# Kernel tuning notes

Measured on AMD Instinct MI355X. Metric: run time of the kernel, lower is better.

The kernel has to match this reference:

```python
import jax, jax.numpy as jnp
import numpy as np

B, IN_DIM, LATENT_DIM, EMBED_DIM = 262144, 512, 128, 10000


def setup_inputs() -> dict:
    key = jax.random.key(0)
    k_x, k_y, k_wlv, k_blv, k_wmu, k_bmu, k_we, k_be = jax.random.split(key, 8)
    s_in = 1.0 / np.sqrt(IN_DIM)
    s_e = 1.0 / np.sqrt(EMBED_DIM)
    return {
        "x": jax.random.normal(k_x, (B, IN_DIM), dtype=jnp.float32),
        "y": jax.random.randint(k_y, (B,), 0, EMBED_DIM, dtype=jnp.int32),
        # torch nn.Linear weights are [out_features, in_features]
        "W_logvar": jax.random.uniform(k_wlv, (LATENT_DIM, IN_DIM), minval=-s_in, maxval=s_in, dtype=jnp.float32),
        "b_logvar": jax.random.uniform(k_blv, (LATENT_DIM,), minval=-s_in, maxval=s_in, dtype=jnp.float32),
        "W_mean": jax.random.uniform(k_wmu, (LATENT_DIM, IN_DIM), minval=-s_in, maxval=s_in, dtype=jnp.float32),
        "b_mean": jax.random.uniform(k_bmu, (LATENT_DIM,), minval=-s_in, maxval=s_in, dtype=jnp.float32),
        "W_embed": jax.random.uniform(k_we, (LATENT_DIM, EMBED_DIM), minval=-s_e, maxval=s_e, dtype=jnp.float32),
        "b_embed": jax.random.uniform(k_be, (LATENT_DIM,), minval=-s_e, maxval=s_e, dtype=jnp.float32),
    }


def reference(x, y, W_logvar, b_logvar, W_mean, b_mean, W_embed, b_embed):
    # logvar / mean heads: plain dense GEMMs, x @ W.T + b
    logvar = jnp.einsum("bi,li->bl", x, W_logvar) + b_logvar
    mean = jnp.einsum("bi,li->bl", x, W_mean) + b_mean
    # one_hot(y) @ W_embed.T + b_embed  ==  gather columns of W_embed at y
    embed = jnp.take(W_embed, y, axis=1).T + b_embed  # [B, latent_dim]
    return (logvar, mean, embed)
```

## Files before the change

### kernel.cpp

```cpp
#include <hip/hip_runtime.h>
#include <hip/hip_bf16.h>

#define NB 262144
#define KD 512
#define ED 10000

typedef __attribute__((ext_vector_type(8))) short s8v;
typedef __attribute__((ext_vector_type(4))) float f4v;

typedef __attribute__((address_space(1))) const unsigned int gu32_t;
typedef __attribute__((address_space(3))) unsigned int lu32_t;

__device__ __forceinline__ short f2bf(float f) {
  union { __hip_bfloat16 h; short s; } u;
  u.h = __float2bfloat16(f);
  return u.s;
}

__global__ void prep_w(const float* __restrict__ Wlv, const float* __restrict__ Wmu,
                       unsigned short* __restrict__ wbf) {
  int i = blockIdx.x * 256 + threadIdx.x;
  int row = i >> 9, col = i & 511;
  float v = (row < 128) ? Wlv[(row << 9) | col] : Wmu[((row - 128) << 9) | col];
  union { __hip_bfloat16 h; unsigned short s; } u;
  u.h = __float2bfloat16(v);
  wbf[i] = u.s;
}

__global__ void prep_embT(const float* __restrict__ We, const float* __restrict__ be,
                          float* __restrict__ embT) {
  int v = blockIdx.x;
  int l = threadIdx.x;
  embT[(size_t)v * 128 + l] = We[(size_t)l * ED + v] + be[l];
}

__global__ __launch_bounds__(512, 4) void gemm_heads(
    const float* __restrict__ x, const unsigned short* __restrict__ wbf,
    const float* __restrict__ blv, const float* __restrict__ bmu,
    float* __restrict__ out) {
  __shared__ char lds[65536];
  const int tid  = threadIdx.x;
  const int lane = tid & 63;
  const int wid  = tid >> 6;
  const int gm   = blockIdx.x << 7;
  const int wm   = wid >> 2;
  const int wn   = wid & 3;

  unsigned xoff[4], woff[4], xdst[4], wdst[4];
#pragma unroll
  for (int c = 0; c < 4; ++c) {
    int o16 = (wid << 8) + (c << 6) + lane;
    {
      int row = o16 >> 4, q16 = o16 & 15;
      int kb16 = q16 ^ ((row & 7) << 1);
      xoff[c] = (unsigned)(row << 9) + (unsigned)(kb16 << 2);
      xdst[c] = (unsigned)(((wid << 8) + (c << 6)) << 4);
    }
    {
      int row = o16 >> 3, q16 = o16 & 7;
      int kb16 = q16 ^ (row & 7);
      woff[c] = (unsigned)(row << 9) + (unsigned)(kb16 << 3);
      wdst[c] = 32768u + (unsigned)(((wid << 8) + (c << 6)) << 4);
    }
  }
  const float* xblk = x + ((size_t)gm << 9);

  unsigned offA[4], offB[4];
#pragma unroll
  for (int t = 0; t < 4; ++t) {
    { int row = (wm << 6) + (t << 4) + (lane & 15);
      int kb  = (lane >> 4) << 5;
      offA[t] = (unsigned)(row << 8) + (unsigned)(kb ^ ((row & 7) << 5)); }
    { int row = (wn << 6) + (t << 4) + (lane & 15);
      int kb  = (lane >> 4) << 4;
      offB[t] = 32768u + (unsigned)(row << 7) + (unsigned)(kb ^ ((row & 7) << 4)); }
  }

  f4v acc[4][4];
#pragma unroll
  for (int i = 0; i < 4; ++i)
#pragma unroll
    for (int j = 0; j < 4; ++j) acc[i][j] = (f4v)0.f;

  for (int ko = 0; ko < 8; ++ko) {
    const int ke = ko << 6;
#pragma unroll
    for (int c = 0; c < 4; ++c) {
      __builtin_amdgcn_global_load_lds((const gu32_t*)(xblk + xoff[c] + ke),
                                       (lu32_t*)(lds + xdst[c]), 16, 0, 0);
      __builtin_amdgcn_global_load_lds((const gu32_t*)(wbf + woff[c] + ke),
                                       (lu32_t*)(lds + wdst[c]), 16, 0, 0);
    }
    __syncthreads();
#pragma unroll
    for (int ks = 0; ks < 2; ++ks) {
      s8v bfr[4];
#pragma unroll
      for (int nt = 0; nt < 4; ++nt)
        bfr[nt] = *(const s8v*)(lds + (offB[nt] ^ (ks << 6)));
#pragma unroll
      for (int mt = 0; mt < 4; ++mt) {
        const char* pa = lds + (offA[mt] ^ (ks << 7));
        float4 a0 = *(const float4*)(pa);
        float4 a1 = *(const float4*)(pa + 16);
        s8v af;
        af[0] = f2bf(a0.x); af[1] = f2bf(a0.y); af[2] = f2bf(a0.z); af[3] = f2bf(a0.w);
        af[4] = f2bf(a1.x); af[5] = f2bf(a1.y); af[6] = f2bf(a1.z); af[7] = f2bf(a1.w);
#pragma unroll
        for (int nt = 0; nt < 4; ++nt)
          acc[mt][nt] = __builtin_amdgcn_mfma_f32_16x16x32_bf16(af, bfr[nt], acc[mt][nt], 0, 0, 0);
      }
    }
    __syncthreads();
  }

  const int col16 = lane & 15;
  const int rsub  = (lane >> 4) << 2;
#pragma unroll
  for (int nt = 0; nt < 4; ++nt) {
    int col = (wn << 6) + (nt << 4) + col16;
    float bias = (col < 128) ? blv[col] : bmu[col - 128];
    float* ob = (col < 128) ? (out + col)
                            : (out + ((size_t)NB << 7) + (col - 128));
#pragma unroll
    for (int mt = 0; mt < 4; ++mt) {
      int row0 = gm + (wm << 6) + (mt << 4) + rsub;
#pragma unroll
      for (int r = 0; r < 4; ++r)
        ob[(size_t)(row0 + r) << 7] = acc[mt][nt][r] + bias;
    }
  }
}

__global__ void embed_fast(const int* __restrict__ y, const float* __restrict__ embT,
                           float* __restrict__ out3) {
  unsigned t = blockIdx.x * 256 + threadIdx.x;
  int b  = t >> 5;
  int l4 = (t & 31) << 2;
  int v  = y[b];
  float4 s = *(const float4*)(embT + (size_t)v * 128 + l4);
  *(float4*)(out3 + ((size_t)b << 7) + l4) = s;
}

__global__ void gemm_naive(const float* __restrict__ x,
                           const float* __restrict__ Wlv, const float* __restrict__ blv,
                           const float* __restrict__ Wmu, const float* __restrict__ bmu,
                           float* __restrict__ out) {
  __shared__ float xr[512];
  int b = blockIdx.x;
  for (int i = threadIdx.x; i < 512; i += 256) xr[i] = x[(size_t)b * 512 + i];
  __syncthreads();
  int c = threadIdx.x;
  const float* w = (c < 128) ? (Wlv + c * 512) : (Wmu + (c - 128) * 512);
  float s = 0.f;
  for (int k = 0; k < 512; ++k) s += xr[k] * w[k];
  s += (c < 128) ? blv[c] : bmu[c - 128];
  float* o = (c < 128) ? (out + (size_t)b * 128 + c)
                       : (out + ((size_t)NB << 7) + (size_t)b * 128 + (c - 128));
  *o = s;
}

__global__ void embed_direct(const int* __restrict__ y, const float* __restrict__ We,
                             const float* __restrict__ be, float* __restrict__ out3) {
  size_t t = (size_t)blockIdx.x * 256 + threadIdx.x;
  int b = (int)(t >> 7), l = (int)(t & 127);
  out3[t] = We[(size_t)l * ED + y[b]] + be[l];
}

extern "C" void kernel_launch(void* const* d_in, const int* in_sizes, int n_in,
                              void* d_out, int out_size, void* d_ws, size_t ws_size,
                              hipStream_t stream) {
  const float* x   = (const float*)d_in[0];
  const int*   y   = (const int*)d_in[1];
  const float* Wlv = (const float*)d_in[2];
  const float* blv = (const float*)d_in[3];
  const float* Wmu = (const float*)d_in[4];
  const float* bmu = (const float*)d_in[5];
  const float* We  = (const float*)d_in[6];
  const float* be  = (const float*)d_in[7];
  float* out  = (float*)d_out;
  float* out3 = out + ((size_t)NB << 8);

  const size_t needW = 256 * 512 * sizeof(unsigned short);
  const size_t needE = needW + (size_t)ED * 128 * sizeof(float);
  unsigned short* wbf = (unsigned short*)d_ws;
  float* embT = (float*)((char*)d_ws + needW);

  if (ws_size >= needW) {
    prep_w<<<512, 256, 0, stream>>>(Wlv, Wmu, wbf);
    gemm_heads<<<NB / 128, 512, 0, stream>>>(x, wbf, blv, bmu, out);
  } else {
    gemm_naive<<<NB, 256, 0, stream>>>(x, Wlv, blv, Wmu, bmu, out);
  }

  if (ws_size >= needE) {
    prep_embT<<<ED, 128, 0, stream>>>(We, be, embT);
    embed_fast<<<NB * 32 / 256, 256, 0, stream>>>(y, embT, out3);
  } else {
    embed_direct<<<NB * 128 / 256, 256, 0, stream>>>(y, We, be, out3);
  }
}
```

Measured before the change: 288.6 us.

## Double-buffer GEMM K-loop with smaller K tiles and tile the embedding transpose

The heads GEMM now uses K-steps of 32 instead of 64, split across two LDS buffers. The next tile's global-to-LDS load is issued before computing on the current tile, so load latency overlaps the MFMA work. Swizzle patterns are recomputed to match the narrower tiles. Separately, the embedding-table transpose now stages 32 columns at a time through a padded shared tile, so both the reads and the writes are coalesced. The catch is that there are now 16 barrier-separated iterations instead of 8.

```diff
diff --git a/kernel.cpp b/kernel.cpp
--- a/kernel.cpp
+++ b/kernel.cpp
@@ -29,9 +29,23 @@
 
 __global__ void prep_embT(const float* __restrict__ We, const float* __restrict__ be,
                           float* __restrict__ embT) {
-  int v = blockIdx.x;
-  int l = threadIdx.x;
-  embT[(size_t)v * 128 + l] = We[(size_t)l * ED + v] + be[l];
+  __shared__ float t[32][129];
+  const int v0 = blockIdx.x << 5;
+#pragma unroll
+  for (int j = 0; j < 16; ++j) {
+    int idx = j * 256 + threadIdx.x;
+    int l = idx >> 5, vi = idx & 31;
+    int v = v0 + vi;
+    t[vi][l] = (v < ED) ? We[(size_t)l * ED + v] : 0.f;
+  }
+  __syncthreads();
+#pragma unroll
+  for (int j = 0; j < 16; ++j) {
+    int idx = j * 256 + threadIdx.x;
+    int v = idx >> 7, l = idx & 127;
+    if (v0 + v < ED)
+      embT[(size_t)(v0 + v) * 128 + l] = t[v][l] + be[l];
+  }
 }
 
 __global__ __launch_bounds__(512, 4) void gemm_heads(
@@ -45,71 +59,76 @@
   const int gm   = blockIdx.x << 7;
   const int wm   = wid >> 2;
   const int wn   = wid & 3;
-
-  unsigned xoff[4], woff[4], xdst[4], wdst[4];
-#pragma unroll
-  for (int c = 0; c < 4; ++c) {
-    int o16 = (wid << 8) + (c << 6) + lane;
-    {
-      int row = o16 >> 4, q16 = o16 & 15;
-      int kb16 = q16 ^ ((row & 7) << 1);
-      xoff[c] = (unsigned)(row << 9) + (unsigned)(kb16 << 2);
-      xdst[c] = (unsigned)(((wid << 8) + (c << 6)) << 4);
+  const float* xblk = x + ((size_t)gm << 9);
+
+  unsigned aSrc[2], aDst[2], bSrc[2], bDst[2];
+#pragma unroll
+  for (int s = 0; s < 2; ++s) {
+    int c = tid + (s << 9);
+    { int row = c >> 3, q = c & 7;
+      int qp = q ^ ((row & 3) << 1);
+      aSrc[s] = (unsigned)(row << 9) + (unsigned)(qp << 2);
+      aDst[s] = (unsigned)(c << 4); }
+    { int row = c >> 2, q = c & 3;
+      int qp = q ^ ((row >> 1) & 3);
+      bSrc[s] = (unsigned)(row << 9) + (unsigned)(qp << 3);
+      bDst[s] = 32768u + (unsigned)(c << 4); }
+  }
+
+  unsigned offA[4], offB[4];
+#pragma unroll
+  for (int t4 = 0; t4 < 4; ++t4) {
+    { int row = (wm << 6) + (t4 << 4) + (lane & 15);
+      int q = ((lane >> 4) << 1) ^ ((row & 3) << 1);
+      offA[t4] = (unsigned)(row << 7) + (unsigned)(q << 4); }
+    { int row = (wn << 6) + (t4 << 4) + (lane & 15);
+      int q = (lane >> 4) ^ ((row >> 1) & 3);
+      offB[t4] = 32768u + (unsigned)(row << 6) + (unsigned)(q << 4); }
+  }
+
+  f4v acc[4][4];
+#pragma unroll
+  for (int i = 0; i < 4; ++i)
+#pragma unroll
+    for (int j = 0; j < 4; ++j) acc[i][j] = (f4v)0.f;
+
+#pragma unroll
+  for (int s = 0; s < 2; ++s) {
+    __builtin_amdgcn_global_load_lds((const gu32_t*)(xblk + aSrc[s]),
+                                     (lu32_t*)(lds + aDst[s]), 16, 0, 0);
+    __builtin_amdgcn_global_load_lds((const gu32_t*)(wbf + bSrc[s]),
+                                     (lu32_t*)(lds + bDst[s]), 16, 0, 0);
+  }
+  __syncthreads();
+
+  for (int t = 0; t < 16; ++t) {
+    const unsigned db = (unsigned)((t & 1) << 14);
+    if (t < 15) {
+      const int ke = (t + 1) << 5;
+      const unsigned db2 = (unsigned)(((t + 1) & 1) << 14);
+#pragma unroll
+      for (int s = 0; s < 2; ++s) {
+        __builtin_amdgcn_global_load_lds((const gu32_t*)(xblk + aSrc[s] + ke),
+                                         (lu32_t*)(lds + aDst[s] + db2), 16, 0, 0);
+        __builtin_amdgcn_global_load_lds((const gu32_t*)(wbf + bSrc[s] + ke),
+                                         (lu32_t*)(lds + bDst[s] + db2), 16, 0, 0);
+      }
     }
-    {
-      int row = o16 >> 3, q16 = o16 & 7;
-      int kb16 = q16 ^ (row & 7);
-      woff[c] = (unsigned)(row << 9) + (unsigned)(kb16 << 3);
-      wdst[c] = 32768u + (unsigned)(((wid << 8) + (c << 6)) << 4);
-    }
-  }
-  const float* xblk = x + ((size_t)gm << 9);
-
-  unsigned offA[4], offB[4];
-#pragma unroll
-  for (int t = 0; t < 4; ++t) {
-    { int row = (wm << 6) + (t << 4) + (lane & 15);
-      int kb  = (lane >> 4) << 5;
-      offA[t] = (unsigned)(row << 8) + (unsigned)(kb ^ ((row & 7) << 5)); }
-    { int row = (wn << 6) + (t << 4) + (lane & 15);
-      int kb  = (lane >> 4) << 4;
-      offB[t] = 32768u + (unsigned)(row << 7) + (unsigned)(kb ^ ((row & 7) << 4)); }
-  }
-
-  f4v acc[4][4];
-#pragma unroll
-  for (int i = 0; i < 4; ++i)
-#pragma unroll
-    for (int j = 0; j < 4; ++j) acc[i][j] = (f4v)0.f;
-
-  for (int ko = 0; ko < 8; ++ko) {
-    const int ke = ko << 6;
-#pragma unroll
-    for (int c = 0; c < 4; ++c) {
-      __builtin_amdgcn_global_load_lds((const gu32_t*)(xblk + xoff[c] + ke),
-                                       (lu32_t*)(lds + xdst[c]), 16, 0, 0);
-      __builtin_amdgcn_global_load_lds((const gu32_t*)(wbf + woff[c] + ke),
-                                       (lu32_t*)(lds + wdst[c]), 16, 0, 0);
-    }
-    __syncthreads();
-#pragma unroll
-    for (int ks = 0; ks < 2; ++ks) {
-      s8v bfr[4];
+    s8v bfr[4];
+#pragma unroll
+    for (int nt = 0; nt < 4; ++nt)
+      bfr[nt] = *(const s8v*)(lds + offB[nt] + db);
+#pragma unroll
+    for (int mt = 0; mt < 4; ++mt) {
+      const char* pa = lds + offA[mt] + db;
+      float4 a0 = *(const float4*)(pa);
+      float4 a1 = *(const float4*)(pa + 16);
+      s8v af;
+      af[0] = f2bf(a0.x); af[1] = f2bf(a0.y); af[2] = f2bf(a0.z); af[3] = f2bf(a0.w);
+      af[4] = f2bf(a1.x); af[5] = f2bf(a1.y); af[6] = f2bf(a1.z); af[7] = f2bf(a1.w);
 #pragma unroll
       for (int nt = 0; nt < 4; ++nt)
-        bfr[nt] = *(const s8v*)(lds + (offB[nt] ^ (ks << 6)));
-#pragma unroll
-      for (int mt = 0; mt < 4; ++mt) {
-        const char* pa = lds + (offA[mt] ^ (ks << 7));
-        float4 a0 = *(const float4*)(pa);
-        float4 a1 = *(const float4*)(pa + 16);
-        s8v af;
-        af[0] = f2bf(a0.x); af[1] = f2bf(a0.y); af[2] = f2bf(a0.z); af[3] = f2bf(a0.w);
-        af[4] = f2bf(a1.x); af[5] = f2bf(a1.y); af[6] = f2bf(a1.z); af[7] = f2bf(a1.w);
-#pragma unroll
-        for (int nt = 0; nt < 4; ++nt)
-          acc[mt][nt] = __builtin_amdgcn_mfma_f32_16x16x32_bf16(af, bfr[nt], acc[mt][nt], 0, 0, 0);
-      }
+        acc[mt][nt] = __builtin_amdgcn_mfma_f32_16x16x32_bf16(af, bfr[nt], acc[mt][nt], 0, 0, 0);
     }
     __syncthreads();
   }
@@ -194,7 +213,7 @@
   }
 
   if (ws_size >= needE) {
-    prep_embT<<<ED, 128, 0, stream>>>(We, be, embT);
+    prep_embT<<<(ED + 31) / 32, 256, 0, stream>>>(We, be, embT);
     embed_fast<<<NB * 32 / 256, 256, 0, stream>>>(y, embT, out3);
   } else {
     embed_direct<<<NB * 128 / 256, 256, 0, stream>>>(y, We, be, out3);
```

New measurement: 315.0 us. +9.2%, slower.
